# Kernel tuning notes

Hardware: AMD Instinct MI355X
Metric: run time of the kernel (lower is better)

## Reference

```python
import jax, jax.numpy as jnp
import numpy as np

B, NNODE, D = 128, 64, 64          # graphs, nodes per graph, invariant feat dim
N = B * NNODE                      # 8192 nodes
E = B * NNODE * (NNODE - 1)        # 516096 directed edges (fully connected per graph)


def _silu(x):
    return x * jax.nn.sigmoid(x)


def _ln(x, w, b, eps=1e-5):
    mu = jnp.mean(x, axis=-1, keepdims=True)
    var = jnp.var(x, axis=-1, keepdims=True)
    return (x - mu) / jnp.sqrt(var + eps) * w + b


def setup_inputs() -> dict:
    key = jax.random.key(0)
    ks = jax.random.split(key, 12)
    # node -> graph assignment, sorted
    batch = np.repeat(np.arange(B), NNODE)
    # fully-connected directed edges within each graph (i != j)
    idx = np.arange(NNODE)
    s, d = np.meshgrid(idx, idx, indexing='ij')
    m = s != d
    s, d = s[m], d[m]
    off = (np.arange(B) * NNODE)[:, None]
    src = (s[None, :] + off).ravel()
    dst = (d[None, :] + off).ravel()
    E_idx = jnp.asarray(np.stack([src, dst]), dtype=jnp.int32)
    return dict(
        batch=jnp.asarray(batch, jnp.int32),
        X=jax.random.normal(ks[0], (N, 3), jnp.float32),
        H=jax.random.normal(ks[1], (N, D), jnp.float32),
        E_idx=E_idx,
        x_norm_w=jnp.ones((1, 1), jnp.float32),
        q_w1=jax.random.normal(ks[2], (D, D), jnp.float32) * 0.05,
        q_w2=jax.random.normal(ks[3], (D, D), jnp.float32) * 0.05,
        kv_w1=jax.random.normal(ks[4], (D + 1, 2 * D), jnp.float32) * 0.05,
        kv_w2=jax.random.normal(ks[5], (2 * D, 2 * D), jnp.float32) * 0.05,
        qn_w=jnp.ones((D,), jnp.float32), qn_b=jnp.zeros((D,), jnp.float32),
        kn_w=jnp.ones((D,), jnp.float32), kn_b=jnp.zeros((D,), jnp.float32),
        phx_w1=jax.random.normal(ks[6], (D, D), jnp.float32) * 0.05,
        phx_w2=jax.random.normal(ks[7], (D, 1), jnp.float32) * 0.05,
        phh_w1=jax.random.normal(ks[8], (D, D), jnp.float32) * 0.05,
        phh_b1=jnp.zeros((D,), jnp.float32),
        phh_w2=jax.random.normal(ks[9], (D, D), jnp.float32) * 0.05,
        phh_b2=jnp.zeros((D,), jnp.float32),
    )


def reference(batch, X, H, E_idx, x_norm_w, q_w1, q_w2, kv_w1, kv_w2,
              qn_w, qn_b, kn_w, kn_b, phx_w1, phx_w2,
              phh_w1, phh_b1, phh_w2, phh_b2):
    src, dst = E_idx[0], E_idx[1]
    # ---- E3Norm: scale positions by per-graph mean norm ----
    norm = jnp.linalg.norm(X, axis=-1, keepdims=True)                 # [N,1]
    cnt = jax.ops.segment_sum(jnp.ones((N,), X.dtype), batch, num_segments=B)
    mean_norm = jax.ops.segment_sum(norm, batch, num_segments=B) / cnt[:, None]
    Xn = x_norm_w * X / (mean_norm[batch] + 1e-5)                     # [N,3]
    # ---- edge gathers + MLPs ----
    Q = _silu(H[dst] @ q_w1) @ q_w2                                   # [E,D]
    rel = Xn[src] - Xn[dst]                                           # [E,3]
    rel_dist = jnp.sum(rel * rel, axis=-1, keepdims=True)             # [E,1]
    X_rel_norm = rel / (1.0 + jnp.sqrt(rel_dist + 1e-8))
    kv_in = jnp.concatenate([rel_dist, H[src]], axis=-1)              # [E,D+1]
    kv = _silu(kv_in @ kv_w1) @ kv_w2                                 # [E,2D]
    K, V = kv[:, :D], kv[:, D:]
    Q = _ln(Q, qn_w, qn_b)
    K = _ln(K, kn_w, kn_b)
    # ---- scatter softmax over incoming edges of dst ----
    scores = jnp.sum(Q * K, axis=-1) / jnp.sqrt(jnp.asarray(D, X.dtype))  # [E]
    m = jax.ops.segment_max(scores, dst, num_segments=N)
    e = jnp.exp(scores - m[dst])
    s = jax.ops.segment_sum(e, dst, num_segments=N)
    alpha = e / s[dst]                                                # [E]
    att = alpha[:, None] * V                                          # [E,D]
    # ---- scatter-sum aggregations ----
    A = jax.ops.segment_sum(att, dst, num_segments=N)                 # [N,D]
    AH = jax.ops.segment_sum(att * H[dst], dst, num_segments=N)       # [N,D]
    phx = _silu(att @ phx_w1) @ phx_w2                                # [E,1]
    X_out = Xn + jax.ops.segment_sum(X_rel_norm * phx, dst, num_segments=N)
    H_out = H + (_silu((A * AH) @ phh_w1 + phh_b1) @ phh_w2 + phh_b2)
    return X_out, H_out
```

## Files before the change

kernel.cpp:

```cpp
#include <hip/hip_runtime.h>
#include <math.h>

#define NB     128
#define NNODE  64
#define NTOT   8192
#define DIM    64
#define PSTR   136
#define WS72   72

typedef __bf16 bf16x8 __attribute__((ext_vector_type(8)));
typedef float  f32x4  __attribute__((ext_vector_type(4)));

__device__ __forceinline__ float frcp(float x) {
    return __builtin_amdgcn_rcpf(x);
}

__device__ __forceinline__ float silu_f(float x) {
    return x * frcp(1.0f + __expf(-x));
}

__device__ __forceinline__ unsigned short bf16bits(float f) {
    return __builtin_bit_cast(unsigned short, (__bf16)f);
}

__device__ __forceinline__ bf16x8 to_bf16x8(const float* v) {
    bf16x8 o;
    #pragma unroll
    for (int j = 0; j < 8; ++j) o[j] = (__bf16)v[j];
    return o;
}

__device__ __forceinline__ float wsum(float v) {
    #pragma unroll
    for (int m = 1; m < 64; m <<= 1) v += __shfl_xor(v, m, 64);
    return v;
}

__global__ __launch_bounds__(256) void k0_prep(
        const float* __restrict__ kvw2, const float* __restrict__ phxw1,
        const float* __restrict__ X, const float* __restrict__ xw,
        const float* __restrict__ qw1, const float* __restrict__ qw2,
        const float* __restrict__ kvw1,
        const float* __restrict__ phh1, const float* __restrict__ phh2,
        unsigned short* __restrict__ w2x, float* __restrict__ Xn4,
        unsigned short* __restrict__ qw1T, unsigned short* __restrict__ qw2T,
        unsigned short* __restrict__ kvw1T,
        unsigned short* __restrict__ phh1T, unsigned short* __restrict__ phh2T) {
    const int k = blockIdx.x;
    const int T = threadIdx.x;
    if (T < 128) {
        w2x[T*PSTR + k] = bf16bits(kvw2[k*128 + T]);
    } else if (T < 192) {
        const int n2 = T - 128;
        float acc = 0.f;
        #pragma unroll 8
        for (int j = 0; j < 64; ++j)
            acc += kvw2[k*128 + 64 + j] * phxw1[j*64 + n2];
        w2x[(128 + n2)*PSTR + k] = bf16bits(acc);
    } else {
        const int L = T - 192;
        const int n = k*64 + L;
        const float x0 = X[n*3+0], x1 = X[n*3+1], x2 = X[n*3+2];
        const float nm = sqrtf(x0*x0 + x1*x1 + x2*x2);
        const float mean = wsum(nm) * (1.0f/64.0f);
        const float sc = xw[0] * frcp(mean + 1e-5f);
        float4 o; o.x = x0*sc; o.y = x1*sc; o.z = x2*sc; o.w = 0.f;
        *(float4*)&Xn4[n*4] = o;
    }
    if (k < 64) {
        if (T < 128) kvw1T[T*WS72 + k] = bf16bits(kvw1[(1+k)*128 + T]);
    } else {
        const int kk = k - 64;
        if (T < 64)       qw1T[T*WS72 + kk]        = bf16bits(qw1[kk*64 + T]);
        else if (T < 128) qw2T[(T-64)*WS72 + kk]   = bf16bits(qw2[kk*64 + (T-64)]);
        else if (T < 192) phh1T[(T-128)*WS72 + kk] = bf16bits(phh1[kk*64 + (T-128)]);
        else              phh2T[(T-192)*WS72 + kk] = bf16bits(phh2[kk*64 + (T-192)]);
    }
}

__global__ __launch_bounds__(128) void k2_node(
        const float* __restrict__ H,
        const unsigned short* __restrict__ qw1T,
        const float* __restrict__ qnw, const float* __restrict__ qnb,
        float* __restrict__ Qn, unsigned short* __restrict__ Ptb) {
    const int nb = blockIdx.x * 32;
    const int T = threadIdx.x, w = T >> 6, L = T & 63;
    const int q = L >> 4, m = L & 15;
    __shared__ __align__(16) unsigned short swt[256*WS72];
    __shared__ __align__(16) unsigned short zb[32*WS72];

    {
        const uint4* s = (const uint4*)qw1T;
        uint4* d = (uint4*)swt;
        #pragma unroll
        for (int it = 0; it < 18; ++it) d[T + 128*it] = s[T + 128*it];
    }

    bf16x8 hf[2];
    #pragma unroll
    for (int ks = 0; ks < 2; ++ks) {
        float v[8];
        *(float4*)&v[0] = *(const float4*)&H[(size_t)(nb + w*16 + m)*64 + ks*32 + q*8];
        *(float4*)&v[4] = *(const float4*)&H[(size_t)(nb + w*16 + m)*64 + ks*32 + q*8 + 4];
        hf[ks] = to_bf16x8(v);
    }
    __syncthreads();

    f32x4 acc[4];
    #pragma unroll
    for (int ct = 0; ct < 4; ++ct) acc[ct] = (f32x4){0.f,0.f,0.f,0.f};
    #pragma unroll
    for (int ks = 0; ks < 2; ++ks)
        #pragma unroll
        for (int ct = 0; ct < 4; ++ct) {
            const bf16x8 b = *(const bf16x8*)&swt[(ct*16 + m)*WS72 + ks*32 + q*8];
            acc[ct] = __builtin_amdgcn_mfma_f32_16x16x32_bf16(hf[ks], b, acc[ct], 0, 0, 0);
        }
    #pragma unroll
    for (int ct = 0; ct < 4; ++ct)
        #pragma unroll
        for (int r = 0; r < 4; ++r)
            zb[(w*16 + q*4 + r)*WS72 + ct*16 + m] = bf16bits(silu_f(acc[ct][r]));
    __syncthreads();

    bf16x8 zf[2];
    #pragma unroll
    for (int ks = 0; ks < 2; ++ks)
        zf[ks] = *(const bf16x8*)&zb[(w*16 + m)*WS72 + ks*32 + q*8];
    #pragma unroll
    for (int ct = 0; ct < 4; ++ct) acc[ct] = (f32x4){0.f,0.f,0.f,0.f};
    #pragma unroll
    for (int ks = 0; ks < 2; ++ks)
        #pragma unroll
        for (int ct = 0; ct < 4; ++ct) {
            const bf16x8 b = *(const bf16x8*)&swt[(64 + ct*16 + m)*WS72 + ks*32 + q*8];
            acc[ct] = __builtin_amdgcn_mfma_f32_16x16x32_bf16(zf[ks], b, acc[ct], 0, 0, 0);
        }
    float qnwv[4], qnbv[4];
    #pragma unroll
    for (int ct = 0; ct < 4; ++ct) { qnwv[ct] = qnw[ct*16+m]; qnbv[ct] = qnb[ct*16+m]; }
    #pragma unroll
    for (int r = 0; r < 4; ++r) {
        float s1 = 0.f, s2 = 0.f;
        #pragma unroll
        for (int ct = 0; ct < 4; ++ct) {
            const float z = acc[ct][r];
            s1 += z; s2 = fmaf(z, z, s2);
        }
        #pragma unroll
        for (int sh = 1; sh < 16; sh <<= 1) {
            s1 += __shfl_xor(s1, sh, 64);
            s2 += __shfl_xor(s2, sh, 64);
        }
        const float mu = s1 * (1.0f/64.0f);
        const float rstd = rsqrtf(s2 * (1.0f/64.0f) - mu*mu + 1e-5f);
        const int row = nb + w*16 + q*4 + r;
        #pragma unroll
        for (int ct = 0; ct < 4; ++ct)
            Qn[(size_t)row*64 + ct*16 + m] = (acc[ct][r] - mu)*rstd*qnwv[ct] + qnbv[ct];
    }

    #pragma unroll
    for (int ph = 0; ph < 2; ++ph) {
        #pragma unroll
        for (int ct = 0; ct < 4; ++ct) acc[ct] = (f32x4){0.f,0.f,0.f,0.f};
        #pragma unroll
        for (int ks = 0; ks < 2; ++ks)
            #pragma unroll
            for (int ct = 0; ct < 4; ++ct) {
                const bf16x8 b = *(const bf16x8*)&swt[(128 + ph*64 + ct*16 + m)*WS72 + ks*32 + q*8];
                acc[ct] = __builtin_amdgcn_mfma_f32_16x16x32_bf16(hf[ks], b, acc[ct], 0, 0, 0);
            }
        #pragma unroll
        for (int ct = 0; ct < 4; ++ct)
            #pragma unroll
            for (int r = 0; r < 4; ++r)
                Ptb[(size_t)(nb + w*16 + q*4 + r)*PSTR + ph*64 + ct*16 + m]
                    = bf16bits(acc[ct][r]);
    }
}

__global__ __launch_bounds__(256, 3) void k3_edge(
        const float* __restrict__ Xn4, const float* __restrict__ Qn,
        const unsigned short* __restrict__ Ptb,
        const unsigned short* __restrict__ w2x,
        const float* __restrict__ kvw1,
        const float* __restrict__ knw, const float* __restrict__ knb,
        const float* __restrict__ pxw2,
        float* __restrict__ Abuf, float* __restrict__ Xout) {
    const int bid = blockIdx.x;
    const int g = bid >> 3, dgrp = bid & 7;
    const int T = threadIdx.x, w = T >> 6, L = T & 63;
    const int q = L >> 4, m = L & 15;
    const int pair = w >> 1, half = w & 1;

    __shared__ __align__(16) unsigned short sw2[128*PSTR];
    __shared__ __align__(16) float sXn[64][4];
    __shared__ __align__(16) float sQn[8][64];
    __shared__ __align__(16) float sxr[4][32][4];
    __shared__ float w0s[128];
    __shared__ float knws[64], knbs[64], pxs[64];
    __shared__ float sred[2][2][2];
    __shared__ float sA[2][64];
    __shared__ float sX[2][4];

    {
        const uint4* s1 = (const uint4*)w2x;
        uint4* d1 = (uint4*)sw2;
        #pragma unroll
        for (int it = 0; it < 9; ++it) {
            const int idx = T + 256*it;
            if (idx < 128*PSTR/8) d1[idx] = s1[idx];
        }
        const float* qsrc = Qn + ((size_t)g*64 + dgrp*8)*64;
        for (int idx = T; idx < 512; idx += 256)
            sQn[idx >> 6][idx & 63] = qsrc[idx];
        if (T < 64) *(float4*)&sXn[T][0] = *(const float4*)&Xn4[(g*64 + T)*4];
        if (T < 128) w0s[T] = kvw1[T];
        if (T < 64)            knws[T]       = knw[T];
        else if (T < 128)      knbs[T - 64]  = knb[T - 64];
        else if (T < 192)      pxs[T - 128]  = pxw2[T - 128];
    }
    __syncthreads();

    const unsigned short* PtG = Ptb + (size_t)g*64*PSTR;
    const unsigned short* Gw  = w2x + 128*PSTR;

    #pragma unroll 1
    for (int i = 0; i < 4; ++i) {
        const int dql = i*2 + pair;
        const int dl  = dgrp*8 + dql;
        const int d   = g*64 + dl;

        if (L < 32) {
            const int row = half*32 + L;
            const float4 xs  = *(const float4*)&sXn[row][0];
            const float4 xdv = *(const float4*)&sXn[dl][0];
            const float r0 = xs.x - xdv.x, r1 = xs.y - xdv.y, r2 = xs.z - xdv.z;
            const float rd = r0*r0 + r1*r1 + r2*r2;
            const float inv = frcp(1.0f + sqrtf(rd + 1e-8f));
            float4 o; o.x = r0*inv; o.y = r1*inv; o.z = r2*inv; o.w = rd;
            *(float4*)&sxr[w][L][0] = o;
        }
        asm volatile("s_waitcnt lgkmcnt(0)" ::: "memory");

        bf16x8 af[2][4];
        float rdv[2];
        #pragma unroll
        for (int rt = 0; rt < 2; ++rt) rdv[rt] = sxr[w][rt*16 + m][3];
        #pragma unroll
        for (int ks = 0; ks < 4; ++ks) {
            float w0v[8];
            *(float4*)&w0v[0] = *(const float4*)&w0s[ks*32 + q*8];
            *(float4*)&w0v[4] = *(const float4*)&w0s[ks*32 + q*8 + 4];
            #pragma unroll
            for (int rt = 0; rt < 2; ++rt) {
                const int row = half*32 + rt*16 + m;
                const bf16x8 pb = *(const bf16x8*)&PtG[(size_t)row*PSTR + ks*32 + q*8];
                bf16x8 o;
                #pragma unroll
                for (int j = 0; j < 8; ++j) {
                    const float pf = (float)pb[j];
                    o[j] = (__bf16)silu_f(fmaf(rdv[rt], w0v[j], pf));
                }
                af[rt][ks] = o;
            }
        }

        f32x4 acc[4][2];

        #pragma unroll
        for (int ct = 0; ct < 4; ++ct)
            #pragma unroll
            for (int rt = 0; rt < 2; ++rt)
                acc[ct][rt] = (f32x4){0.f, 0.f, 0.f, 0.f};
        #pragma unroll
        for (int ks = 0; ks < 4; ++ks)
            #pragma unroll
            for (int ct = 0; ct < 4; ++ct) {
                const bf16x8 b = *(const bf16x8*)&sw2[(ct*16 + m)*PSTR + ks*32 + q*8];
                #pragma unroll
                for (int rt = 0; rt < 2; ++rt)
                    acc[ct][rt] = __builtin_amdgcn_mfma_f32_16x16x32_bf16(
                                      af[rt][ks], b, acc[ct][rt], 0, 0, 0);
            }

        float qdw[4], Sqdw = 0.f, Sqdb = 0.f;
        #pragma unroll
        for (int ct = 0; ct < 4; ++ct) {
            const float qd = sQn[dql][ct*16 + m];
            qdw[ct] = qd * knws[ct*16 + m];
            Sqdw += qdw[ct];
            Sqdb += qd * knbs[ct*16 + m];
        }
        #pragma unroll
        for (int sh = 1; sh < 16; sh <<= 1) {
            Sqdw += __shfl_xor(Sqdw, sh, 64);
            Sqdb += __shfl_xor(Sqdb, sh, 64);
        }
        float sc[2][4];
        #pragma unroll
        for (int rt = 0; rt < 2; ++rt)
            #pragma unroll
            for (int r = 0; r < 4; ++r) {
                float s1 = 0.f, s2 = 0.f, skq = 0.f;
                #pragma unroll
                for (int ct = 0; ct < 4; ++ct) {
                    const float kv = acc[ct][rt][r];
                    s1 += kv; s2 = fmaf(kv, kv, s2); skq = fmaf(kv, qdw[ct], skq);
                }
                #pragma unroll
                for (int sh = 1; sh < 16; sh <<= 1) {
                    s1  += __shfl_xor(s1,  sh, 64);
                    s2  += __shfl_xor(s2,  sh, 64);
                    skq += __shfl_xor(skq, sh, 64);
                }
                const float mu = s1 * (1.0f/64.0f);
                const float rstd = rsqrtf(s2 * (1.0f/64.0f) - mu*mu + 1e-5f);
                const float scv = (rstd * (skq - mu*Sqdw) + Sqdb) * 0.125f;
                const int row_g = half*32 + rt*16 + q*4 + r;
                sc[rt][r] = (row_g == dl) ? -1e30f : scv;
            }

        float mx = -1e30f;
        #pragma unroll
        for (int rt = 0; rt < 2; ++rt)
            #pragma unroll
            for (int r = 0; r < 4; ++r) mx = fmaxf(mx, sc[rt][r]);
        mx = fmaxf(mx, __shfl_xor(mx, 16, 64));
        mx = fmaxf(mx, __shfl_xor(mx, 32, 64));
        float al[2][4], S = 0.f;
        #pragma unroll
        for (int rt = 0; rt < 2; ++rt)
            #pragma unroll
            for (int r = 0; r < 4; ++r) {
                al[rt][r] = __expf(sc[rt][r] - mx);
                S += al[rt][r];
            }
        S += __shfl_xor(S, 16, 64);
        S += __shfl_xor(S, 32, 64);
        if (L == 0) { sred[pair][half][0] = mx; sred[pair][half][1] = S; }
        __syncthreads();
        {
            const float mo = sred[pair][half^1][0];
            const float So = sred[pair][half^1][1];
            const float M  = fmaxf(mx, mo);
            const float es = __expf(mx - M);
            const float eo = __expf(mo - M);
            const float alf = es * frcp(S*es + So*eo);
            #pragma unroll
            for (int rt = 0; rt < 2; ++rt)
                #pragma unroll
                for (int r = 0; r < 4; ++r) al[rt][r] *= alf;
        }

        #pragma unroll
        for (int ct = 0; ct < 4; ++ct)
            #pragma unroll
            for (int rt = 0; rt < 2; ++rt)
                acc[ct][rt] = (f32x4){0.f, 0.f, 0.f, 0.f};
        #pragma unroll
        for (int ks = 0; ks < 4; ++ks)
            #pragma unroll
            for (int ct = 0; ct < 4; ++ct) {
                const bf16x8 b = *(const bf16x8*)&sw2[(64 + ct*16 + m)*PSTR + ks*32 + q*8];
                #pragma unroll
                for (int rt = 0; rt < 2; ++rt)
                    acc[ct][rt] = __builtin_amdgcn_mfma_f32_16x16x32_bf16(
                                      af[rt][ks], b, acc[ct][rt], 0, 0, 0);
            }
        float p[4];
        #pragma unroll
        for (int ct = 0; ct < 4; ++ct) {
            float pv = 0.f;
            #pragma unroll
            for (int rt = 0; rt < 2; ++rt)
                #pragma unroll
                for (int r = 0; r < 4; ++r)
                    pv = fmaf(al[rt][r], acc[ct][rt][r], pv);
            pv += __shfl_xor(pv, 16, 64);
            pv += __shfl_xor(pv, 32, 64);
            p[ct] = pv;
        }
        if (half == 1 && q == 0)
            #pragma unroll
            for (int ct = 0; ct < 4; ++ct) sA[pair][ct*16 + m] = p[ct];
        __syncthreads();
        if (half == 0 && q == 0)
            #pragma unroll
            for (int ct = 0; ct < 4; ++ct)
                Abuf[(size_t)d*64 + ct*16 + m] = p[ct] + sA[pair][ct*16 + m];

        #pragma unroll
        for (int ct = 0; ct < 4; ++ct)
            #pragma unroll
            for (int rt = 0; rt < 2; ++rt)
                acc[ct][rt] = (f32x4){0.f, 0.f, 0.f, 0.f};
        #pragma unroll
        for (int ks = 0; ks < 4; ++ks)
            #pragma unroll
            for (int ct = 0; ct < 4; ++ct) {
                const bf16x8 b = *(const bf16x8*)&Gw[(size_t)(ct*16 + m)*PSTR + ks*32 + q*8];
                #pragma unroll
                for (int rt = 0; rt < 2; ++rt)
                    acc[ct][rt] = __builtin_amdgcn_mfma_f32_16x16x32_bf16(
                                      af[rt][ks], b, acc[ct][rt], 0, 0, 0);
            }

        float pxc[4];
        #pragma unroll
        for (int ct = 0; ct < 4; ++ct) pxc[ct] = pxs[ct*16 + m];
        float xa0 = 0.f, xa1 = 0.f, xa2 = 0.f;
        #pragma unroll
        for (int rt = 0; rt < 2; ++rt)
            #pragma unroll
            for (int r = 0; r < 4; ++r) {
                float ph = 0.f;
                #pragma unroll
                for (int ct = 0; ct < 4; ++ct)
                    ph = fmaf(silu_f(al[rt][r] * acc[ct][rt][r]), pxc[ct], ph);
                #pragma unroll
                for (int sh = 1; sh < 16; sh <<= 1) ph += __shfl_xor(ph, sh, 64);
                const float4 xr = *(const float4*)&sxr[w][rt*16 + q*4 + r][0];
                xa0 = fmaf(ph, xr.x, xa0);
                xa1 = fmaf(ph, xr.y, xa1);
                xa2 = fmaf(ph, xr.z, xa2);
            }
        xa0 += __shfl_xor(xa0, 16, 64); xa0 += __shfl_xor(xa0, 32, 64);
        xa1 += __shfl_xor(xa1, 16, 64); xa1 += __shfl_xor(xa1, 32, 64);
        xa2 += __shfl_xor(xa2, 16, 64); xa2 += __shfl_xor(xa2, 32, 64);
        if (half == 1 && L == 0) {
            sX[pair][0] = xa0; sX[pair][1] = xa1; sX[pair][2] = xa2;
        }
        __syncthreads();
        if (half == 0 && L == 0) {
            const float4 xdv = *(const float4*)&sXn[dl][0];
            Xout[(size_t)d*3 + 0] = xdv.x + xa0 + sX[pair][0];
            Xout[(size_t)d*3 + 1] = xdv.y + xa1 + sX[pair][1];
            Xout[(size_t)d*3 + 2] = xdv.z + xa2 + sX[pair][2];
        }
    }
}

__global__ __launch_bounds__(128) void k4_hout(
        const float* __restrict__ H, const float* __restrict__ Abuf,
        const unsigned short* __restrict__ phh1T, const float* __restrict__ b1,
        const float* __restrict__ b2, float* __restrict__ Hout) {
    const int nb = blockIdx.x * 32;
    const int T = threadIdx.x, w = T >> 6, L = T & 63;
    const int q = L >> 4, m = L & 15;
    __shared__ __align__(16) unsigned short swt[128*WS72];
    __shared__ __align__(16) unsigned short zb[32*WS72];

    {
        const uint4* s = (const uint4*)phh1T;
        uint4* d = (uint4*)swt;
        #pragma unroll
        for (int it = 0; it < 9; ++it) d[T + 128*it] = s[T + 128*it];
    }

    bf16x8 uf[2];
    #pragma unroll
    for (int ks = 0; ks < 2; ++ks) {
        const size_t base = (size_t)(nb + w*16 + m)*64 + ks*32 + q*8;
        float a[8], h[8], v[8];
        *(float4*)&a[0] = *(const float4*)&Abuf[base];
        *(float4*)&a[4] = *(const float4*)&Abuf[base + 4];
        *(float4*)&h[0] = *(const float4*)&H[base];
        *(float4*)&h[4] = *(const float4*)&H[base + 4];
        #pragma unroll
        for (int j = 0; j < 8; ++j) v[j] = a[j]*a[j]*h[j];
        uf[ks] = to_bf16x8(v);
    }
    __syncthreads();

    f32x4 acc[4];
    #pragma unroll
    for (int ct = 0; ct < 4; ++ct) acc[ct] = (f32x4){0.f,0.f,0.f,0.f};
    #pragma unroll
    for (int ks = 0; ks < 2; ++ks)
        #pragma unroll
        for (int ct = 0; ct < 4; ++ct) {
            const bf16x8 b = *(const bf16x8*)&swt[(ct*16 + m)*WS72 + ks*32 + q*8];
            acc[ct] = __builtin_amdgcn_mfma_f32_16x16x32_bf16(uf[ks], b, acc[ct], 0, 0, 0);
        }
    #pragma unroll
    for (int ct = 0; ct < 4; ++ct) {
        const float bv = b1[ct*16 + m];
        #pragma unroll
        for (int r = 0; r < 4; ++r)
            zb[(w*16 + q*4 + r)*WS72 + ct*16 + m] = bf16bits(silu_f(acc[ct][r] + bv));
    }
    __syncthreads();

    bf16x8 zf[2];
    #pragma unroll
    for (int ks = 0; ks < 2; ++ks)
        zf[ks] = *(const bf16x8*)&zb[(w*16 + m)*WS72 + ks*32 + q*8];
    #pragma unroll
    for (int ct = 0; ct < 4; ++ct) acc[ct] = (f32x4){0.f,0.f,0.f,0.f};
    #pragma unroll
    for (int ks = 0; ks < 2; ++ks)
        #pragma unroll
        for (int ct = 0; ct < 4; ++ct) {
            const bf16x8 b = *(const bf16x8*)&swt[(64 + ct*16 + m)*WS72 + ks*32 + q*8];
            acc[ct] = __builtin_amdgcn_mfma_f32_16x16x32_bf16(zf[ks], b, acc[ct], 0, 0, 0);
        }
    #pragma unroll
    for (int ct = 0; ct < 4; ++ct) {
        const float bv = b2[ct*16 + m];
        #pragma unroll
        for (int r = 0; r < 4; ++r) {
            const size_t idx = (size_t)(nb + w*16 + q*4 + r)*64 + ct*16 + m;
            Hout[idx] = H[idx] + acc[ct][r] + bv;
        }
    }
}

extern "C" void kernel_launch(void* const* d_in, const int* in_sizes, int n_in,
                              void* d_out, int out_size, void* d_ws, size_t ws_size,
                              hipStream_t stream) {
    const float* X    = (const float*)d_in[1];
    const float* H    = (const float*)d_in[2];
    const float* xw   = (const float*)d_in[4];
    const float* qw1  = (const float*)d_in[5];
    const float* qw2  = (const float*)d_in[6];
    const float* kvw1 = (const float*)d_in[7];
    const float* kvw2 = (const float*)d_in[8];
    const float* qnw  = (const float*)d_in[9];
    const float* qnb  = (const float*)d_in[10];
    const float* knw  = (const float*)d_in[11];
    const float* knb  = (const float*)d_in[12];
    const float* pxw1 = (const float*)d_in[13];
    const float* pxw2 = (const float*)d_in[14];
    const float* phw1 = (const float*)d_in[15];
    const float* phb1 = (const float*)d_in[16];
    const float* phw2 = (const float*)d_in[17];
    const float* phb2 = (const float*)d_in[18];

    float* out = (float*)d_out;
    char*  ws  = (char*)d_ws;

    size_t off = 0;
    float* Xn4 = (float*)(ws + off);          off += (size_t)NTOT*4*4;
    float* Qn  = (float*)(ws + off);          off += (size_t)NTOT*64*4;
    unsigned short* Ptb = (unsigned short*)(ws + off); off += (size_t)NTOT*PSTR*2;
    float* Ab  = (float*)(ws + off);          off += (size_t)NTOT*64*4;
    unsigned short* w2x   = (unsigned short*)(ws + off); off += (size_t)192*PSTR*2;
    unsigned short* qw1T  = (unsigned short*)(ws + off); off += (size_t)64*WS72*2;
    unsigned short* qw2T  = (unsigned short*)(ws + off); off += (size_t)64*WS72*2;
    unsigned short* kvw1T = (unsigned short*)(ws + off); off += (size_t)128*WS72*2;
    unsigned short* phh1T = (unsigned short*)(ws + off); off += (size_t)64*WS72*2;
    unsigned short* phh2T = (unsigned short*)(ws + off); off += (size_t)64*WS72*2;

    k0_prep<<<128, 256, 0, stream>>>(kvw2, pxw1, X, xw, qw1, qw2, kvw1,
                                     phw1, phw2, w2x, Xn4,
                                     qw1T, qw2T, kvw1T, phh1T, phh2T);
    k2_node<<<256, 128, 0, stream>>>(H, qw1T, qnw, qnb, Qn, Ptb);
    k3_edge<<<1024, 256, 0, stream>>>(Xn4, Qn, Ptb, w2x, kvw1, knw, knb,
                                      pxw2, Ab, out);
    k4_hout<<<256, 128, 0, stream>>>(H, Ab, phh1T, phb1, phb2, out + NTOT*3);
}
```

Measured before the change: 184.9 us.

## Split node kernels into single-wave blocks, use DPP row reductions, merge edge-kernel barriers

k2_node and k4_hout now run one wave per block over 16 rows. They read weights directly from global memory instead of staging them in LDS, and the __syncthreads are gone. k2_node splits the Q path and the K/V-projection path across two block roles to expose more parallelism. In k3_edge, the 16-lane shuffle reductions become DPP row_shr adds with a swizzle broadcast of lane 15, and the two per-destination barriers for Abuf and Xout are merged into one. Risks are more global and L2 weight traffic, and correctness depends on the lane-15 convention for the DPP sums.

```diff
diff --git a/kernel.cpp b/kernel.cpp
--- a/kernel.cpp
+++ b/kernel.cpp
@@ -34,6 +34,24 @@
     #pragma unroll
     for (int m = 1; m < 64; m <<= 1) v += __shfl_xor(v, m, 64);
     return v;
+}
+
+template<int CTRL>
+__device__ __forceinline__ float dpp_add(float v) {
+    const int r = __builtin_amdgcn_update_dpp(
+        0, __builtin_bit_cast(int, v), CTRL, 0xF, 0xF, true);
+    return v + __builtin_bit_cast(float, r);
+}
+__device__ __forceinline__ float row_sum16(float v) {
+    v = dpp_add<0x111>(v);
+    v = dpp_add<0x112>(v);
+    v = dpp_add<0x114>(v);
+    v = dpp_add<0x118>(v);
+    return v;
+}
+__device__ __forceinline__ float bcast15(float v) {
+    return __builtin_bit_cast(float,
+        __builtin_amdgcn_ds_swizzle(__builtin_bit_cast(int, v), 0x01F0));
 }
 
 __global__ __launch_bounds__(256) void k0_prep(
@@ -78,62 +96,76 @@
     }
 }
 
-__global__ __launch_bounds__(128) void k2_node(
+__global__ __launch_bounds__(64) void k2_node(
         const float* __restrict__ H,
-        const unsigned short* __restrict__ qw1T,
+        const unsigned short* __restrict__ wbase,
         const float* __restrict__ qnw, const float* __restrict__ qnb,
         float* __restrict__ Qn, unsigned short* __restrict__ Ptb) {
-    const int nb = blockIdx.x * 32;
-    const int T = threadIdx.x, w = T >> 6, L = T & 63;
-    const int q = L >> 4, m = L & 15;
-    __shared__ __align__(16) unsigned short swt[256*WS72];
-    __shared__ __align__(16) unsigned short zb[32*WS72];
-
-    {
-        const uint4* s = (const uint4*)qw1T;
-        uint4* d = (uint4*)swt;
-        #pragma unroll
-        for (int it = 0; it < 18; ++it) d[T + 128*it] = s[T + 128*it];
-    }
+    const int tile = blockIdx.x >> 1, role = blockIdx.x & 1;
+    const int nb = tile * 16;
+    const int L = threadIdx.x, q = L >> 4, m = L & 15;
+    __shared__ __align__(16) unsigned short zb[16*WS72];
 
     bf16x8 hf[2];
     #pragma unroll
     for (int ks = 0; ks < 2; ++ks) {
         float v[8];
-        *(float4*)&v[0] = *(const float4*)&H[(size_t)(nb + w*16 + m)*64 + ks*32 + q*8];
-        *(float4*)&v[4] = *(const float4*)&H[(size_t)(nb + w*16 + m)*64 + ks*32 + q*8 + 4];
+        *(float4*)&v[0] = *(const float4*)&H[(size_t)(nb + m)*64 + ks*32 + q*8];
+        *(float4*)&v[4] = *(const float4*)&H[(size_t)(nb + m)*64 + ks*32 + q*8 + 4];
         hf[ks] = to_bf16x8(v);
     }
-    __syncthreads();
 
     f32x4 acc[4];
+    if (role == 1) {
+        const unsigned short* kvw1T = wbase + 128*WS72;
+        #pragma unroll
+        for (int ph = 0; ph < 2; ++ph) {
+            #pragma unroll
+            for (int ct = 0; ct < 4; ++ct) acc[ct] = (f32x4){0.f,0.f,0.f,0.f};
+            #pragma unroll
+            for (int ks = 0; ks < 2; ++ks)
+                #pragma unroll
+                for (int ct = 0; ct < 4; ++ct) {
+                    const bf16x8 b = *(const bf16x8*)&kvw1T[(ph*64 + ct*16 + m)*WS72 + ks*32 + q*8];
+                    acc[ct] = __builtin_amdgcn_mfma_f32_16x16x32_bf16(hf[ks], b, acc[ct], 0, 0, 0);
+                }
+            #pragma unroll
+            for (int ct = 0; ct < 4; ++ct)
+                #pragma unroll
+                for (int r = 0; r < 4; ++r)
+                    Ptb[(size_t)(nb + q*4 + r)*PSTR + ph*64 + ct*16 + m]
+                        = bf16bits(acc[ct][r]);
+        }
+        return;
+    }
+
     #pragma unroll
     for (int ct = 0; ct < 4; ++ct) acc[ct] = (f32x4){0.f,0.f,0.f,0.f};
     #pragma unroll
     for (int ks = 0; ks < 2; ++ks)
         #pragma unroll
         for (int ct = 0; ct < 4; ++ct) {
-            const bf16x8 b = *(const bf16x8*)&swt[(ct*16 + m)*WS72 + ks*32 + q*8];
+            const bf16x8 b = *(const bf16x8*)&wbase[(ct*16 + m)*WS72 + ks*32 + q*8];
             acc[ct] = __builtin_amdgcn_mfma_f32_16x16x32_bf16(hf[ks], b, acc[ct], 0, 0, 0);
         }
     #pragma unroll
     for (int ct = 0; ct < 4; ++ct)
         #pragma unroll
         for (int r = 0; r < 4; ++r)
-            zb[(w*16 + q*4 + r)*WS72 + ct*16 + m] = bf16bits(silu_f(acc[ct][r]));
-    __syncthreads();
+            zb[(q*4 + r)*WS72 + ct*16 + m] = bf16bits(silu_f(acc[ct][r]));
 
     bf16x8 zf[2];
     #pragma unroll
     for (int ks = 0; ks < 2; ++ks)
-        zf[ks] = *(const bf16x8*)&zb[(w*16 + m)*WS72 + ks*32 + q*8];
+        zf[ks] = *(const bf16x8*)&zb[m*WS72 + ks*32 + q*8];
+    const unsigned short* qw2T = wbase + 64*WS72;
     #pragma unroll
     for (int ct = 0; ct < 4; ++ct) acc[ct] = (f32x4){0.f,0.f,0.f,0.f};
     #pragma unroll
     for (int ks = 0; ks < 2; ++ks)
         #pragma unroll
         for (int ct = 0; ct < 4; ++ct) {
-            const bf16x8 b = *(const bf16x8*)&swt[(64 + ct*16 + m)*WS72 + ks*32 + q*8];
+            const bf16x8 b = *(const bf16x8*)&qw2T[(ct*16 + m)*WS72 + ks*32 + q*8];
             acc[ct] = __builtin_amdgcn_mfma_f32_16x16x32_bf16(zf[ks], b, acc[ct], 0, 0, 0);
         }
     float qnwv[4], qnbv[4];
@@ -154,29 +186,10 @@
         }
         const float mu = s1 * (1.0f/64.0f);
         const float rstd = rsqrtf(s2 * (1.0f/64.0f) - mu*mu + 1e-5f);
-        const int row = nb + w*16 + q*4 + r;
+        const int row = nb + q*4 + r;
         #pragma unroll
         for (int ct = 0; ct < 4; ++ct)
             Qn[(size_t)row*64 + ct*16 + m] = (acc[ct][r] - mu)*rstd*qnwv[ct] + qnbv[ct];
-    }
-
-    #pragma unroll
-    for (int ph = 0; ph < 2; ++ph) {
-        #pragma unroll
-        for (int ct = 0; ct < 4; ++ct) acc[ct] = (f32x4){0.f,0.f,0.f,0.f};
-        #pragma unroll
-        for (int ks = 0; ks < 2; ++ks)
-            #pragma unroll
-            for (int ct = 0; ct < 4; ++ct) {
-                const bf16x8 b = *(const bf16x8*)&swt[(128 + ph*64 + ct*16 + m)*WS72 + ks*32 + q*8];
-                acc[ct] = __builtin_amdgcn_mfma_f32_16x16x32_bf16(hf[ks], b, acc[ct], 0, 0, 0);
-            }
-        #pragma unroll
-        for (int ct = 0; ct < 4; ++ct)
-            #pragma unroll
-            for (int r = 0; r < 4; ++r)
-                Ptb[(size_t)(nb + w*16 + q*4 + r)*PSTR + ph*64 + ct*16 + m]
-                    = bf16bits(acc[ct][r]);
     }
 }
 
@@ -225,6 +238,7 @@
 
     const unsigned short* PtG = Ptb + (size_t)g*64*PSTR;
     const unsigned short* Gw  = w2x + 128*PSTR;
+    const float mflag = (m == 15) ? 1.0f : 0.0f;
 
     #pragma unroll 1
     for (int i = 0; i < 4; ++i) {
@@ -293,11 +307,8 @@
             Sqdw += qdw[ct];
             Sqdb += qd * knbs[ct*16 + m];
         }
-        #pragma unroll
-        for (int sh = 1; sh < 16; sh <<= 1) {
-            Sqdw += __shfl_xor(Sqdw, sh, 64);
-            Sqdb += __shfl_xor(Sqdb, sh, 64);
-        }
+        Sqdw = row_sum16(Sqdw);
+        Sqdb = row_sum16(Sqdb);
         float sc[2][4];
         #pragma unroll
         for (int rt = 0; rt < 2; ++rt)
@@ -309,15 +320,13 @@
                     const float kv = acc[ct][rt][r];
                     s1 += kv; s2 = fmaf(kv, kv, s2); skq = fmaf(kv, qdw[ct], skq);
                 }
-                #pragma unroll
-                for (int sh = 1; sh < 16; sh <<= 1) {
-                    s1  += __shfl_xor(s1,  sh, 64);
-                    s2  += __shfl_xor(s2,  sh, 64);
-                    skq += __shfl_xor(skq, sh, 64);
-                }
+                s1  = row_sum16(s1);
+                s2  = row_sum16(s2);
+                skq = row_sum16(skq);
                 const float mu = s1 * (1.0f/64.0f);
                 const float rstd = rsqrtf(s2 * (1.0f/64.0f) - mu*mu + 1e-5f);
-                const float scv = (rstd * (skq - mu*Sqdw) + Sqdb) * 0.125f;
+                float scv = (rstd * (skq - mu*Sqdw) + Sqdb) * 0.125f;
+                scv = bcast15(scv);
                 const int row_g = half*32 + rt*16 + q*4 + r;
                 sc[rt][r] = (row_g == dl) ? -1e30f : scv;
             }
@@ -382,14 +391,6 @@
             pv += __shfl_xor(pv, 32, 64);
             p[ct] = pv;
         }
-        if (half == 1 && q == 0)
-            #pragma unroll
-            for (int ct = 0; ct < 4; ++ct) sA[pair][ct*16 + m] = p[ct];
-        __syncthreads();
-        if (half == 0 && q == 0)
-            #pragma unroll
-            for (int ct = 0; ct < 4; ++ct)
-                Abuf[(size_t)d*64 + ct*16 + m] = p[ct] + sA[pair][ct*16 + m];
 
         #pragma unroll
         for (int ct = 0; ct < 4; ++ct)
@@ -419,8 +420,7 @@
                 #pragma unroll
                 for (int ct = 0; ct < 4; ++ct)
                     ph = fmaf(silu_f(al[rt][r] * acc[ct][rt][r]), pxc[ct], ph);
-                #pragma unroll
-                for (int sh = 1; sh < 16; sh <<= 1) ph += __shfl_xor(ph, sh, 64);
+                ph = row_sum16(ph) * mflag;
                 const float4 xr = *(const float4*)&sxr[w][rt*16 + q*4 + r][0];
                 xa0 = fmaf(ph, xr.x, xa0);
                 xa1 = fmaf(ph, xr.y, xa1);
@@ -429,40 +429,44 @@
         xa0 += __shfl_xor(xa0, 16, 64); xa0 += __shfl_xor(xa0, 32, 64);
         xa1 += __shfl_xor(xa1, 16, 64); xa1 += __shfl_xor(xa1, 32, 64);
         xa2 += __shfl_xor(xa2, 16, 64); xa2 += __shfl_xor(xa2, 32, 64);
-        if (half == 1 && L == 0) {
-            sX[pair][0] = xa0; sX[pair][1] = xa1; sX[pair][2] = xa2;
+
+        if (half == 1) {
+            if (q == 0)
+                #pragma unroll
+                for (int ct = 0; ct < 4; ++ct) sA[pair][ct*16 + m] = p[ct];
+            if (L == 15) {
+                sX[pair][0] = xa0; sX[pair][1] = xa1; sX[pair][2] = xa2;
+            }
         }
         __syncthreads();
-        if (half == 0 && L == 0) {
-            const float4 xdv = *(const float4*)&sXn[dl][0];
-            Xout[(size_t)d*3 + 0] = xdv.x + xa0 + sX[pair][0];
-            Xout[(size_t)d*3 + 1] = xdv.y + xa1 + sX[pair][1];
-            Xout[(size_t)d*3 + 2] = xdv.z + xa2 + sX[pair][2];
-        }
-    }
-}
-
-__global__ __launch_bounds__(128) void k4_hout(
+        if (half == 0) {
+            if (q == 0)
+                #pragma unroll
+                for (int ct = 0; ct < 4; ++ct)
+                    Abuf[(size_t)d*64 + ct*16 + m] = p[ct] + sA[pair][ct*16 + m];
+            if (L == 15) {
+                const float4 xdv = *(const float4*)&sXn[dl][0];
+                Xout[(size_t)d*3 + 0] = xdv.x + xa0 + sX[pair][0];
+                Xout[(size_t)d*3 + 1] = xdv.y + xa1 + sX[pair][1];
+                Xout[(size_t)d*3 + 2] = xdv.z + xa2 + sX[pair][2];
+            }
+        }
+    }
+}
+
+__global__ __launch_bounds__(64) void k4_hout(
         const float* __restrict__ H, const float* __restrict__ Abuf,
-        const unsigned short* __restrict__ phh1T, const float* __restrict__ b1,
-        const float* __restrict__ b2, float* __restrict__ Hout) {
-    const int nb = blockIdx.x * 32;
-    const int T = threadIdx.x, w = T >> 6, L = T & 63;
-    const int q = L >> 4, m = L & 15;
-    __shared__ __align__(16) unsigned short swt[128*WS72];
-    __shared__ __align__(16) unsigned short zb[32*WS72];
-
-    {
-        const uint4* s = (const uint4*)phh1T;
-        uint4* d = (uint4*)swt;
-        #pragma unroll
-        for (int it = 0; it < 9; ++it) d[T + 128*it] = s[T + 128*it];
-    }
+        const unsigned short* __restrict__ wbase,
+        const float* __restrict__ b1, const float* __restrict__ b2,
+        float* __restrict__ Hout) {
+    const int nb = blockIdx.x * 16;
+    const int L = threadIdx.x, q = L >> 4, m = L & 15;
+    __shared__ __align__(16) unsigned short zb[16*WS72];
 
     bf16x8 uf[2];
     #pragma unroll
     for (int ks = 0; ks < 2; ++ks) {
-        const size_t base = (size_t)(nb + w*16 + m)*64 + ks*32 + q*8;
+        const size_t base = (size_t)(nb + m)*64 + ks*32 + q*8;
         float a[8], h[8], v[8];
         *(float4*)&a[0] = *(const float4*)&Abuf[base];
         *(float4*)&a[4] = *(const float4*)&Abuf[base + 4];
@@ -472,7 +476,6 @@
         for (int j = 0; j < 8; ++j) v[j] = a[j]*a[j]*h[j];
         uf[ks] = to_bf16x8(v);
     }
-    __syncthreads();
 
     f32x4 acc[4];
     #pragma unroll
@@ -481,7 +484,7 @@
     for (int ks = 0; ks < 2; ++ks)
         #pragma unroll
         for (int ct = 0; ct < 4; ++ct) {
-            const bf16x8 b = *(const bf16x8*)&swt[(ct*16 + m)*WS72 + ks*32 + q*8];
+            const bf16x8 b = *(const bf16x8*)&wbase[(ct*16 + m)*WS72 + ks*32 + q*8];
             acc[ct] = __builtin_amdgcn_mfma_f32_16x16x32_bf16(uf[ks], b, acc[ct], 0, 0, 0);
         }
     #pragma unroll
@@ -489,21 +492,21 @@
         const float bv = b1[ct*16 + m];
         #pragma unroll
         for (int r = 0; r < 4; ++r)
-            zb[(w*16 + q*4 + r)*WS72 + ct*16 + m] = bf16bits(silu_f(acc[ct][r] + bv));
-    }
-    __syncthreads();
+            zb[(q*4 + r)*WS72 + ct*16 + m] = bf16bits(silu_f(acc[ct][r] + bv));
+    }
 
     bf16x8 zf[2];
     #pragma unroll
     for (int ks = 0; ks < 2; ++ks)
-        zf[ks] = *(const bf16x8*)&zb[(w*16 + m)*WS72 + ks*32 + q*8];
+        zf[ks] = *(const bf16x8*)&zb[m*WS72 + ks*32 + q*8];
+    const unsigned short* phh2T = wbase + 64*WS72;
     #pragma unroll
     for (int ct = 0; ct < 4; ++ct) acc[ct] = (f32x4){0.f,0.f,0.f,0.f};
     #pragma unroll
     for (int ks = 0; ks < 2; ++ks)
         #pragma unroll
         for (int ct = 0; ct < 4; ++ct) {
-            const bf16x8 b = *(const bf16x8*)&swt[(64 + ct*16 + m)*WS72 + ks*32 + q*8];
+            const bf16x8 b = *(const bf16x8*)&phh2T[(ct*16 + m)*WS72 + ks*32 + q*8];
             acc[ct] = __builtin_amdgcn_mfma_f32_16x16x32_bf16(zf[ks], b, acc[ct], 0, 0, 0);
         }
     #pragma unroll
@@ -511,7 +514,7 @@
         const float bv = b2[ct*16 + m];
         #pragma unroll
         for (int r = 0; r < 4; ++r) {
-            const size_t idx = (size_t)(nb + w*16 + q*4 + r)*64 + ct*16 + m;
+            const size_t idx = (size_t)(nb + q*4 + r)*64 + ct*16 + m;
             Hout[idx] = H[idx] + acc[ct][r] + bv;
         }
     }
@@ -556,8 +559,8 @@
     k0_prep<<<128, 256, 0, stream>>>(kvw2, pxw1, X, xw, qw1, qw2, kvw1,
                                      phw1, phw2, w2x, Xn4,
                                      qw1T, qw2T, kvw1T, phh1T, phh2T);
-    k2_node<<<256, 128, 0, stream>>>(H, qw1T, qnw, qnb, Qn, Ptb);
+    k2_node<<<1024, 64, 0, stream>>>(H, qw1T, qnw, qnb, Qn, Ptb);
     k3_edge<<<1024, 256, 0, stream>>>(Xn4, Qn, Ptb, w2x, kvw1, knw, knb,
                                       pxw2, Ab, out);
-    k4_hout<<<256, 128, 0, stream>>>(H, Ab, phh1T, phb1, phb2, out + NTOT*3);
-}
+    k4_hout<<<512, 64, 0, stream>>>(H, Ab, phh1T, phb1, phb2, out + NTOT*3);
+}
```

New measurement: 173.1 us. 6.3% less time.
